# Kernel tuning notes

Hardware: AMD Instinct MI355X
Metric: run time of the kernel (lower is better)

Reference implementation:

```python
import jax, jax.numpy as jnp
import numpy as np
from math import pi

FC_IN, FC_OUT = 64, 64
LABEL_NC = 35
B, C, H, W = 2, 64, 128, 128
EPS = 1e-5
SLOPE = 0.01  # torch leaky_relu default


def _pa(h, w):
    # absolute normalized coordinates, matches init_pos buffers
    xs = (jnp.arange(h, dtype=jnp.float32) / h) * 2.0 - 1.0
    ys = (jnp.arange(w, dtype=jnp.float32) / w) * 2.0 - 1.0
    px = jnp.broadcast_to(xs[:, None], (h, w))
    py = jnp.broadcast_to(ys[None, :], (h, w))
    return jnp.stack([px, py], 0)  # (2,h,w)


def _coords(h, w):
    # f0=3; while-loop runs once (f=3 -> f=1), so exactly 4 channels
    f = 3.0
    ang_x = 2.0 * pi * jnp.remainder(jnp.arange(w, dtype=jnp.float32), f) / f
    ang_y = 2.0 * pi * jnp.remainder(jnp.arange(h, dtype=jnp.float32), f) / f
    xcos = jnp.broadcast_to(jnp.cos(ang_x)[None, :], (h, w))
    xsin = jnp.broadcast_to(jnp.sin(ang_x)[None, :], (h, w))
    ycos = jnp.broadcast_to(jnp.cos(ang_y)[:, None], (h, w))
    ysin = jnp.broadcast_to(jnp.sin(ang_y)[:, None], (h, w))
    return jnp.stack([xcos, xsin, ycos, ysin], 0)  # (4,h,w)


def _nearest(t, h, w):
    # F.interpolate(mode='nearest') index map: floor(i*in/out)
    ih = jnp.arange(h) * t.shape[2] // h
    iw = jnp.arange(w) * t.shape[3] // w
    return t[:, :, ih][:, :, :, iw]


def setup_inputs() -> dict:
    key = jax.random.key(0)
    ks = jax.random.split(key, 7)
    return {
        "x": jax.random.normal(ks[0], (B, C, H, W), jnp.float32),
        "layout": jax.random.normal(ks[1], (B, LABEL_NC, H, W), jnp.float32),
        "pr": jax.random.normal(ks[2], (B, 2, H, W), jnp.float32),
        "conv_w": jax.random.normal(ks[3], (1, 10), jnp.float32) * 0.02,
        "conv_b": jnp.zeros((1,), jnp.float32),
        "W_table": jax.random.normal(ks[4], (LABEL_NC, FC_IN * FC_OUT), jnp.float32),
        "b_table": jax.random.normal(ks[5], (LABEL_NC, FC_OUT), jnp.float32) * 0.02,
        "pl": jax.random.normal(ks[6], (2, H, W), jnp.float32),
    }


def reference(x, layout, pr, conv_w, conv_b, W_table, b_table, pl):
    b, c, h, w = x.shape
    pa = jnp.broadcast_to(_pa(h, w)[None], (b, 2, h, w))
    plb = jnp.broadcast_to(pl[None], (b, 2, h, w))
    coords = jnp.broadcast_to(_coords(h, w)[None], (b, 4, h, w))
    prr = _nearest(pr, h, w)
    pos = jnp.concatenate([pa, plb, prr, coords], axis=1)  # (B,10,h,w)
    # 1x1 conv to a single channel, broadcast-added over C
    x = x + jnp.einsum('bchw,oc->bohw', pos, conv_w) + conv_b[None, :, None, None]
    # argmax-routed per-pixel affine params
    lay = _nearest(layout, h, w)
    arg = jnp.argmax(lay, axis=1)  # (B,h,w) int
    Wg = W_table[arg].reshape(b, h, w, FC_IN, FC_OUT)  # huge gathered tensor (as in original)
    bg = b_table[arg]  # (B,h,w,FC_OUT)
    xh = jnp.transpose(x, (0, 2, 3, 1))  # (B,h,w,C)
    y = jnp.einsum('bhwc,bhwco->bhwo', xh, Wg) + bg
    y = jnp.transpose(y, (0, 3, 1, 2))  # (B,FC_OUT,h,w)
    # instance norm (no affine, biased variance, eps=1e-5)
    mu = jnp.mean(y, axis=(2, 3), keepdims=True)
    var = jnp.var(y, axis=(2, 3), keepdims=True)
    y = (y - mu) * jax.lax.rsqrt(var + EPS)
    return jnp.where(y >= 0, y, SLOPE * y)
```

## Files before the change

kernel.cpp:

```cpp
#include <hip/hip_runtime.h>

#define HH 128
#define WW 128
#define CC 64
#define OO 64
#define NC 35
#define NPIX (HH*WW)
#define NBLK 1024

__global__ __launch_bounds__(256) void ky_kernel(
    const float* __restrict__ x, const float* __restrict__ layout,
    const float* __restrict__ pr, const float* __restrict__ cw,
    const float* __restrict__ cb, const float* __restrict__ Wt,
    const float* __restrict__ bt, const float* __restrict__ pl,
    float* __restrict__ out, float* __restrict__ psum, float* __restrict__ pss)
{
    __shared__ float s_xh[64*33];
    __shared__ float s_y[64*33];
    __shared__ float s_s[32];
    __shared__ int   s_arg[32];
    __shared__ float s_red[4][64][2];

    const int t    = threadIdx.x;
    const int wv   = t >> 6;
    const int lane = t & 63;
    const int i15  = lane & 15;
    const int ihi  = lane >> 4;
    const int tile = blockIdx.x;
    const int b    = tile >> 9;
    const int rem  = tile & 511;
    const int h    = rem >> 2;
    const int w0   = (rem & 3) << 5;

    if (wv == 0 && lane < 32) {
        int w = w0 + lane;
        float pxv = (float)h * (2.0f/128.0f) - 1.0f;
        float pyv = (float)w * (2.0f/128.0f) - 1.0f;
        float pl0 = pl[h*WW + w];
        float pl1 = pl[NPIX + h*WW + w];
        float pr0 = pr[((b*2+0)*HH + h)*WW + w];
        float pr1 = pr[((b*2+1)*HH + h)*WW + w];
        int kx = w % 3, kyy = h % 3;
        const float C1 = -0.5f, S1 = 0.86602540378443864676f;
        float xcv = (kx==0)  ? 1.0f : C1;
        float xsv = (kx==0)  ? 0.0f : ((kx==1)  ? S1 : -S1);
        float ycv = (kyy==0) ? 1.0f : C1;
        float ysv = (kyy==0) ? 0.0f : ((kyy==1) ? S1 : -S1);
        s_s[lane] = cb[0] + pxv*cw[0] + pyv*cw[1] + pl0*cw[2] + pl1*cw[3]
                  + pr0*cw[4] + pr1*cw[5] + xcv*cw[6] + xsv*cw[7]
                  + ycv*cw[8] + ysv*cw[9];
    }

    if (wv == 1 && lane < 32) {
        int w = w0 + lane;
        const float* lp = layout + ((size_t)(b*NC)*HH + h)*WW + w;
        float best = lp[0]; int bi = 0;
        #pragma unroll
        for (int c = 1; c < NC; ++c) {
            float v = lp[(size_t)c*NPIX];
            if (v > best) { best = v; bi = c; }
        }
        s_arg[lane] = bi;
    }

    {
        int p = t & 31, c0 = t >> 5;
        const float* xp = x + ((size_t)(b*CC)*HH + h)*WW + w0 + p;
        #pragma unroll
        for (int k = 0; k < 8; ++k) {
            int c = c0 + 8*k;
            s_xh[c*33 + p] = xp[(size_t)c*NPIX];
        }
    }
    __syncthreads();

    float4 sumv = {0,0,0,0}, ssv = {0,0,0,0};
    for (int i = 0; i < 8; ++i) {
        int p = wv*8 + i;
        int l = s_arg[p];
        float sp = s_s[p];
        const float4* W4 = (const float4*)(Wt + l*4096) + lane;
        float4 a = {0,0,0,0};
        #pragma unroll
        for (int tt = 0; tt < 16; ++tt) {
            float4 q  = W4[tt*64];
            float  xv = s_xh[(4*tt + ihi)*33 + p] + sp;
            a.x = fmaf(xv, q.x, a.x);
            a.y = fmaf(xv, q.y, a.y);
            a.z = fmaf(xv, q.z, a.z);
            a.w = fmaf(xv, q.w, a.w);
        }
        a.x += __shfl_xor(a.x, 16); a.y += __shfl_xor(a.y, 16);
        a.z += __shfl_xor(a.z, 16); a.w += __shfl_xor(a.w, 16);
        a.x += __shfl_xor(a.x, 32); a.y += __shfl_xor(a.y, 32);
        a.z += __shfl_xor(a.z, 32); a.w += __shfl_xor(a.w, 32);
        if (ihi == 0) {
            float4 bq = ((const float4*)(bt + l*64))[i15];
            float y0 = a.x + bq.x, y1 = a.y + bq.y;
            float y2 = a.z + bq.z, y3 = a.w + bq.w;
            int o = 4*i15;
            s_y[(o+0)*33 + p] = y0;
            s_y[(o+1)*33 + p] = y1;
            s_y[(o+2)*33 + p] = y2;
            s_y[(o+3)*33 + p] = y3;
            sumv.x += y0; ssv.x += y0*y0;
            sumv.y += y1; ssv.y += y1*y1;
            sumv.z += y2; ssv.z += y2*y2;
            sumv.w += y3; ssv.w += y3*y3;
        }
    }
    if (ihi == 0) {
        int o = 4*i15;
        s_red[wv][o+0][0] = sumv.x; s_red[wv][o+0][1] = ssv.x;
        s_red[wv][o+1][0] = sumv.y; s_red[wv][o+1][1] = ssv.y;
        s_red[wv][o+2][0] = sumv.z; s_red[wv][o+2][1] = ssv.z;
        s_red[wv][o+3][0] = sumv.w; s_red[wv][o+3][1] = ssv.w;
    }
    __syncthreads();

    {
        int p = t & 31, o0 = t >> 5;
        float* op = out + ((size_t)(b*OO)*HH + h)*WW + w0 + p;
        #pragma unroll
        for (int k = 0; k < 8; ++k) {
            int o = o0 + 8*k;
            op[(size_t)o*NPIX] = s_y[o*33 + p];
        }
    }

    if (wv == 0) {
        float S  = s_red[0][lane][0] + s_red[1][lane][0] + s_red[2][lane][0] + s_red[3][lane][0];
        float SS = s_red[0][lane][1] + s_red[1][lane][1] + s_red[2][lane][1] + s_red[3][lane][1];
        psum[lane*NBLK + tile] = S;
        pss [lane*NBLK + tile] = SS;
    }
}

__global__ __launch_bounds__(256) void stats_kernel(
    const float* __restrict__ psum, const float* __restrict__ pss,
    float* __restrict__ stats)
{
    __shared__ float2 red[256];
    int e = blockIdx.x;
    int b = e >> 6, o = e & 63;
    int t = threadIdx.x;
    const float* ps = psum + o*NBLK + b*512;
    const float* pq = pss  + o*NBLK + b*512;
    float2 v;
    v.x = ps[t] + ps[t+256];
    v.y = pq[t] + pq[t+256];
    red[t] = v;
    __syncthreads();
    #pragma unroll
    for (int s = 128; s > 0; s >>= 1) {
        if (t < s) { red[t].x += red[t+s].x; red[t].y += red[t+s].y; }
        __syncthreads();
    }
    if (t == 0) {
        const float invN = 1.0f/16384.0f;
        float mean = red[0].x * invN;
        float var  = red[0].y * invN - mean*mean;
        stats[e*2+0] = mean;
        stats[e*2+1] = rsqrtf(var + 1e-5f);
    }
}

__global__ __launch_bounds__(256) void norm_kernel(
    float* __restrict__ out, const float* __restrict__ stats)
{
    int idx = blockIdx.x * 256 + threadIdx.x;
    float4* o4 = reinterpret_cast<float4*>(out);
    float4 v = o4[idx];
    int bo = idx >> 12;
    float mean = stats[bo*2 + 0];
    float r    = stats[bo*2 + 1];
    float a;
    a = (v.x - mean) * r; v.x = (a >= 0.f) ? a : 0.01f*a;
    a = (v.y - mean) * r; v.y = (a >= 0.f) ? a : 0.01f*a;
    a = (v.z - mean) * r; v.z = (a >= 0.f) ? a : 0.01f*a;
    a = (v.w - mean) * r; v.w = (a >= 0.f) ? a : 0.01f*a;
    o4[idx] = v;
}

extern "C" void kernel_launch(void* const* d_in, const int* in_sizes, int n_in,
                              void* d_out, int out_size, void* d_ws, size_t ws_size,
                              hipStream_t stream) {
    const float* x      = (const float*)d_in[0];
    const float* layout = (const float*)d_in[1];
    const float* pr     = (const float*)d_in[2];
    const float* cw     = (const float*)d_in[3];
    const float* cb     = (const float*)d_in[4];
    const float* Wt     = (const float*)d_in[5];
    const float* bt     = (const float*)d_in[6];
    const float* pl     = (const float*)d_in[7];
    float* out   = (float*)d_out;
    float* psum  = (float*)d_ws;
    float* pss   = psum + (size_t)OO*NBLK;
    float* stats = pss  + (size_t)OO*NBLK;

    ky_kernel<<<NBLK, 256, 0, stream>>>(x, layout, pr, cw, cb, Wt, bt, pl, out, psum, pss);
    stats_kernel<<<128, 256, 0, stream>>>(psum, pss, stats);
    norm_kernel<<<2048, 256, 0, stream>>>(out, stats);
}
```

Before: 103.1 us.

## Bucket pixels by routed label and run per-bucket register-blocked matvec

```diff
diff --git a/kernel.cpp b/kernel.cpp
--- a/kernel.cpp
+++ b/kernel.cpp
@@ -6,26 +6,24 @@
 #define OO 64
 #define NC 35
 #define NPIX (HH*WW)
-#define NBLK 1024
-
-__global__ __launch_bounds__(256) void ky_kernel(
+#define LISTST NPIX
+#define NBKT (2*NC)
+#define MV_WAVES 2048
+
+
+__global__ __launch_bounds__(256) void prep_kernel(
     const float* __restrict__ x, const float* __restrict__ layout,
     const float* __restrict__ pr, const float* __restrict__ cw,
-    const float* __restrict__ cb, const float* __restrict__ Wt,
-    const float* __restrict__ bt, const float* __restrict__ pl,
-    float* __restrict__ out, float* __restrict__ psum, float* __restrict__ pss)
+    const float* __restrict__ cb, const float* __restrict__ pl,
+    float* __restrict__ xT, int* __restrict__ cnt, int* __restrict__ list)
 {
     __shared__ float s_xh[64*33];
-    __shared__ float s_y[64*33];
     __shared__ float s_s[32];
     __shared__ int   s_arg[32];
-    __shared__ float s_red[4][64][2];
 
     const int t    = threadIdx.x;
     const int wv   = t >> 6;
     const int lane = t & 63;
-    const int i15  = lane & 15;
-    const int ihi  = lane >> 4;
     const int tile = blockIdx.x;
     const int b    = tile >> 9;
     const int rem  = tile & 511;
@@ -74,112 +72,201 @@
     }
     __syncthreads();
 
-    float4 sumv = {0,0,0,0}, ssv = {0,0,0,0};
-    for (int i = 0; i < 8; ++i) {
-        int p = wv*8 + i;
-        int l = s_arg[p];
+    {
+        int p = t >> 3, c0 = (t & 7) << 3;
         float sp = s_s[p];
-        const float4* W4 = (const float4*)(Wt + l*4096) + lane;
-        float4 a = {0,0,0,0};
-        #pragma unroll
-        for (int tt = 0; tt < 16; ++tt) {
-            float4 q  = W4[tt*64];
-            float  xv = s_xh[(4*tt + ihi)*33 + p] + sp;
-            a.x = fmaf(xv, q.x, a.x);
-            a.y = fmaf(xv, q.y, a.y);
-            a.z = fmaf(xv, q.z, a.z);
-            a.w = fmaf(xv, q.w, a.w);
-        }
-        a.x += __shfl_xor(a.x, 16); a.y += __shfl_xor(a.y, 16);
-        a.z += __shfl_xor(a.z, 16); a.w += __shfl_xor(a.w, 16);
-        a.x += __shfl_xor(a.x, 32); a.y += __shfl_xor(a.y, 32);
-        a.z += __shfl_xor(a.z, 32); a.w += __shfl_xor(a.w, 32);
-        if (ihi == 0) {
-            float4 bq = ((const float4*)(bt + l*64))[i15];
-            float y0 = a.x + bq.x, y1 = a.y + bq.y;
-            float y2 = a.z + bq.z, y3 = a.w + bq.w;
-            int o = 4*i15;
-            s_y[(o+0)*33 + p] = y0;
-            s_y[(o+1)*33 + p] = y1;
-            s_y[(o+2)*33 + p] = y2;
-            s_y[(o+3)*33 + p] = y3;
-            sumv.x += y0; ssv.x += y0*y0;
-            sumv.y += y1; ssv.y += y1*y1;
-            sumv.z += y2; ssv.z += y2*y2;
-            sumv.w += y3; ssv.w += y3*y3;
-        }
-    }
-    if (ihi == 0) {
-        int o = 4*i15;
-        s_red[wv][o+0][0] = sumv.x; s_red[wv][o+0][1] = ssv.x;
-        s_red[wv][o+1][0] = sumv.y; s_red[wv][o+1][1] = ssv.y;
-        s_red[wv][o+2][0] = sumv.z; s_red[wv][o+2][1] = ssv.z;
-        s_red[wv][o+3][0] = sumv.w; s_red[wv][o+3][1] = ssv.w;
+        float4 a, d;
+        a.x = s_xh[(c0+0)*33+p] + sp;
+        a.y = s_xh[(c0+1)*33+p] + sp;
+        a.z = s_xh[(c0+2)*33+p] + sp;
+        a.w = s_xh[(c0+3)*33+p] + sp;
+        d.x = s_xh[(c0+4)*33+p] + sp;
+        d.y = s_xh[(c0+5)*33+p] + sp;
+        d.z = s_xh[(c0+6)*33+p] + sp;
+        d.w = s_xh[(c0+7)*33+p] + sp;
+        float* dst = xT + (((size_t)b*NPIX + h*WW + w0 + p) << 6) + c0;
+        *(float4*)dst       = a;
+        *(float4*)(dst + 4) = d;
+    }
+
+    if (t < 32) {
+        int l   = s_arg[t];
+        int bkt = b*NC + l;
+        int idx = atomicAdd(&cnt[bkt], 1);
+        list[bkt*LISTST + idx] = h*WW + w0 + t;
+    }
+}
+
+__global__ __launch_bounds__(256, 2) void mv_kernel(
+    const float* __restrict__ Wt, const float* __restrict__ bt,
+    const float* __restrict__ xT, const int* __restrict__ cnt,
+    const int* __restrict__ list, float* __restrict__ yT,
+    float* __restrict__ gsum, float* __restrict__ gss)
+{
+    const int t    = threadIdx.x;
+    const int lane = t & 63;
+    const int wgid = __builtin_amdgcn_readfirstlane(blockIdx.x * 4 + (t >> 6));
+
+    int c1 = cnt[(lane < NBKT) ? lane : (NBKT-1)];
+    int c2 = cnt[(lane < (NBKT-64)) ? 64 + lane : (NBKT-1)];
+    int m  = c1 > c2 ? c1 : c2;
+    #pragma unroll
+    for (int d_ = 32; d_ >= 1; d_ >>= 1) {
+        int o = __shfl_xor(m, d_);
+        m = m > o ? m : o;
+    }
+    const int maxch = __builtin_amdgcn_readfirstlane((m + 63) >> 6);
+    const int ntask = 2 * NBKT * maxch;
+
+    for (int task = wgid; task < ntask; task += MV_WAVES) {
+        const int half  = task & 1;
+        const int vc    = task >> 1;
+        const int bkt   = vc % NBKT;
+        const int chunk = vc / NBKT;
+        const int n     = cnt[bkt];
+        const int base  = chunk << 6;
+        if (base >= n) continue;
+        const int b = (bkt >= NC) ? 1 : 0;
+        const int l = bkt - b * NC;
+
+        const int  pi    = base + lane;
+        const bool valid = pi < n;
+        const float mask = valid ? 1.0f : 0.0f;
+        const int  pib   = list[bkt*LISTST + (valid ? pi : base)];
+
+        const float* __restrict__ xp = xT + (((size_t)b*NPIX + pib) << 6);
+        float xh[64];
+        #pragma unroll
+        for (int q = 0; q < 16; ++q) {
+            float4 v = ((const float4*)xp)[q];
+            xh[4*q+0] = v.x * mask;
+            xh[4*q+1] = v.y * mask;
+            xh[4*q+2] = v.z * mask;
+            xh[4*q+3] = v.w * mask;
+        }
+
+        const float* __restrict__ Wl = Wt + (size_t)l * 4096;
+        const float* __restrict__ bl = bt + l * 64;
+
+        #pragma unroll
+        for (int pp = 0; pp < 2; ++pp) {
+            const int o0 = (half << 5) + (pp << 4);
+            float acc[16];
+            #pragma unroll
+            for (int k = 0; k < 16; ++k) acc[k] = 0.0f;
+            #pragma unroll
+            for (int c = 0; c < 64; ++c) {
+                const float xv = xh[c];
+                const float4* __restrict__ wr = (const float4*)(Wl + c*64 + o0);
+                float4 wa = wr[0], wb = wr[1], wc = wr[2], wd = wr[3];
+                acc[ 0] = fmaf(xv, wa.x, acc[ 0]);
+                acc[ 1] = fmaf(xv, wa.y, acc[ 1]);
+                acc[ 2] = fmaf(xv, wa.z, acc[ 2]);
+                acc[ 3] = fmaf(xv, wa.w, acc[ 3]);
+                acc[ 4] = fmaf(xv, wb.x, acc[ 4]);
+                acc[ 5] = fmaf(xv, wb.y, acc[ 5]);
+                acc[ 6] = fmaf(xv, wb.z, acc[ 6]);
+                acc[ 7] = fmaf(xv, wb.w, acc[ 7]);
+                acc[ 8] = fmaf(xv, wc.x, acc[ 8]);
+                acc[ 9] = fmaf(xv, wc.y, acc[ 9]);
+                acc[10] = fmaf(xv, wc.z, acc[10]);
+                acc[11] = fmaf(xv, wc.w, acc[11]);
+                acc[12] = fmaf(xv, wd.x, acc[12]);
+                acc[13] = fmaf(xv, wd.y, acc[13]);
+                acc[14] = fmaf(xv, wd.z, acc[14]);
+                acc[15] = fmaf(xv, wd.w, acc[15]);
+            }
+            float y[16];
+            #pragma unroll
+            for (int q = 0; q < 4; ++q) {
+                float4 bb = ((const float4*)(bl + o0))[q];
+                y[4*q+0] = (acc[4*q+0] + bb.x) * mask;
+                y[4*q+1] = (acc[4*q+1] + bb.y) * mask;
+                y[4*q+2] = (acc[4*q+2] + bb.z) * mask;
+                y[4*q+3] = (acc[4*q+3] + bb.w) * mask;
+            }
+            if (valid) {
+                float* __restrict__ yp = yT + (((size_t)b*NPIX + pib) << 6) + o0;
+                ((float4*)yp)[0] = make_float4(y[ 0], y[ 1], y[ 2], y[ 3]);
+                ((float4*)yp)[1] = make_float4(y[ 4], y[ 5], y[ 6], y[ 7]);
+                ((float4*)yp)[2] = make_float4(y[ 8], y[ 9], y[10], y[11]);
+                ((float4*)yp)[3] = make_float4(y[12], y[13], y[14], y[15]);
+            }
+            #pragma unroll
+            for (int k = 0; k < 16; ++k) {
+                float sv = y[k];
+                float sq = y[k]*y[k];
+                #pragma unroll
+                for (int d_ = 32; d_ >= 1; d_ >>= 1) {
+                    sv += __shfl_xor(sv, d_);
+                    sq += __shfl_xor(sq, d_);
+                }
+                if (lane == 0) {
+                    atomicAdd(&gsum[(b<<6) + o0 + k], sv);
+                    atomicAdd(&gss [(b<<6) + o0 + k], sq);
+                }
+            }
+        }
+    }
+}
+
+__global__ __launch_bounds__(256) void norm_kernel(
+    const float* __restrict__ yT, const float* __restrict__ gsum,
+    const float* __restrict__ gss, float* __restrict__ out)
+{
+    __shared__ float s_t[64*65];
+    __shared__ float s_mean[64];
+    __shared__ float s_rstd[64];
+
+    const int t    = threadIdx.x;
+    const int tile = blockIdx.x;
+    const int b    = tile >> 8;
+    const int rem  = tile & 255;
+    const int h    = rem >> 1;
+    const int w0   = (rem & 1) << 6;
+
+    if (t < 64) {
+        const float invN = 1.0f/16384.0f;
+        float mean = gsum[(b<<6)+t] * invN;
+        float var  = gss [(b<<6)+t] * invN - mean*mean;
+        s_mean[t] = mean;
+        s_rstd[t] = rsqrtf(var + 1e-5f);
+    }
+    {
+        const int p = t >> 2, q = t & 3;
+        const float4* yp = (const float4*)(yT + (((size_t)b*NPIX + h*WW + w0 + p) << 6) + (q << 4));
+        #pragma unroll
+        for (int j = 0; j < 4; ++j) {
+            float4 v = yp[j];
+            int o = (q << 4) + (j << 2);
+            s_t[(o+0)*65 + p] = v.x;
+            s_t[(o+1)*65 + p] = v.y;
+            s_t[(o+2)*65 + p] = v.z;
+            s_t[(o+3)*65 + p] = v.w;
+        }
     }
     __syncthreads();
-
-    {
-        int p = t & 31, o0 = t >> 5;
-        float* op = out + ((size_t)(b*OO)*HH + h)*WW + w0 + p;
-        #pragma unroll
-        for (int k = 0; k < 8; ++k) {
-            int o = o0 + 8*k;
-            op[(size_t)o*NPIX] = s_y[o*33 + p];
-        }
-    }
-
-    if (wv == 0) {
-        float S  = s_red[0][lane][0] + s_red[1][lane][0] + s_red[2][lane][0] + s_red[3][lane][0];
-        float SS = s_red[0][lane][1] + s_red[1][lane][1] + s_red[2][lane][1] + s_red[3][lane][1];
-        psum[lane*NBLK + tile] = S;
-        pss [lane*NBLK + tile] = SS;
-    }
-}
-
-__global__ __launch_bounds__(256) void stats_kernel(
-    const float* __restrict__ psum, const float* __restrict__ pss,
-    float* __restrict__ stats)
-{
-    __shared__ float2 red[256];
-    int e = blockIdx.x;
-    int b = e >> 6, o = e & 63;
-    int t = threadIdx.x;
-    const float* ps = psum + o*NBLK + b*512;
-    const float* pq = pss  + o*NBLK + b*512;
-    float2 v;
-    v.x = ps[t] + ps[t+256];
-    v.y = pq[t] + pq[t+256];
-    red[t] = v;
-    __syncthreads();
-    #pragma unroll
-    for (int s = 128; s > 0; s >>= 1) {
-        if (t < s) { red[t].x += red[t+s].x; red[t].y += red[t+s].y; }
-        __syncthreads();
-    }
-    if (t == 0) {
-        const float invN = 1.0f/16384.0f;
-        float mean = red[0].x * invN;
-        float var  = red[0].y * invN - mean*mean;
-        stats[e*2+0] = mean;
-        stats[e*2+1] = rsqrtf(var + 1e-5f);
-    }
-}
-
-__global__ __launch_bounds__(256) void norm_kernel(
-    float* __restrict__ out, const float* __restrict__ stats)
-{
-    int idx = blockIdx.x * 256 + threadIdx.x;
-    float4* o4 = reinterpret_cast<float4*>(out);
-    float4 v = o4[idx];
-    int bo = idx >> 12;
-    float mean = stats[bo*2 + 0];
-    float r    = stats[bo*2 + 1];
-    float a;
-    a = (v.x - mean) * r; v.x = (a >= 0.f) ? a : 0.01f*a;
-    a = (v.y - mean) * r; v.y = (a >= 0.f) ? a : 0.01f*a;
-    a = (v.z - mean) * r; v.z = (a >= 0.f) ? a : 0.01f*a;
-    a = (v.w - mean) * r; v.w = (a >= 0.f) ? a : 0.01f*a;
-    o4[idx] = v;
+    {
+        const int o = t >> 2, q = t & 3;
+        const float mean = s_mean[o];
+        const float r    = s_rstd[o];
+        float* op = out + (((size_t)(b*OO + o)*HH + h)*WW) + w0 + (q << 4);
+        #pragma unroll
+        for (int j = 0; j < 4; ++j) {
+            int wq = (q << 4) + (j << 2);
+            float4 v;
+            v.x = s_t[o*65 + wq + 0];
+            v.y = s_t[o*65 + wq + 1];
+            v.z = s_t[o*65 + wq + 2];
+            v.w = s_t[o*65 + wq + 3];
+            float a_;
+            a_ = (v.x - mean) * r; v.x = (a_ >= 0.f) ? a_ : 0.01f*a_;
+            a_ = (v.y - mean) * r; v.y = (a_ >= 0.f) ? a_ : 0.01f*a_;
+            a_ = (v.z - mean) * r; v.z = (a_ >= 0.f) ? a_ : 0.01f*a_;
+            a_ = (v.w - mean) * r; v.w = (a_ >= 0.f) ? a_ : 0.01f*a_;
+            ((float4*)op)[j] = v;
+        }
+    }
 }
 
 extern "C" void kernel_launch(void* const* d_in, const int* in_sizes, int n_in,
@@ -193,12 +280,18 @@
     const float* Wt     = (const float*)d_in[5];
     const float* bt     = (const float*)d_in[6];
     const float* pl     = (const float*)d_in[7];
-    float* out   = (float*)d_out;
-    float* psum  = (float*)d_ws;
-    float* pss   = psum + (size_t)OO*NBLK;
-    float* stats = pss  + (size_t)OO*NBLK;
-
-    ky_kernel<<<NBLK, 256, 0, stream>>>(x, layout, pr, cw, cb, Wt, bt, pl, out, psum, pss);
-    stats_kernel<<<128, 256, 0, stream>>>(psum, pss, stats);
-    norm_kernel<<<2048, 256, 0, stream>>>(out, stats);
-}
+    float* out = (float*)d_out;
+
+    char*  ws   = (char*)d_ws;
+    int*   cnt  = (int*)ws;
+    float* gsum = (float*)(ws + 1024);
+    float* gss  = (float*)(ws + 2048);
+    int*   list = (int*)(ws + 4096);
+    float* xT   = (float*)(ws + (8u  << 20));
+    float* yT   = (float*)(ws + (16u << 20));
+
+    hipMemsetAsync(d_ws, 0, 4096, stream);
+    prep_kernel<<<1024, 256, 0, stream>>>(x, layout, pr, cw, cb, pl, xT, cnt, list);
+    mv_kernel  <<< 512, 256, 0, stream>>>(Wt, bt, xT, cnt, list, yT, gsum, gss);
+    norm_kernel<<< 512, 256, 0, stream>>>(yT, gsum, gss, out);
+}
```

New measurement: 266.0 us. +158.0%, slower.
